# Performance work log

Measured on AMD Instinct MI355X. Metric: run time of the kernel, lower is better.

Reference implementation:

```python
import jax, jax.numpy as jnp
import numpy as np

# Layer geometry (matches init_kwargs): input_dims=[16,32,16] -> F=16 filters, S=32*16=512 shifts; O=32 output filters
F = 16
S = 512
O = 32
B = 256


def setup_inputs() -> dict:
    key = jax.random.key(0)
    k1, k2, k3 = jax.random.split(key, 3)
    x = jax.random.normal(k1, (B, S * F), dtype=jnp.float32)
    W = jax.random.normal(k2, (S * F, O), dtype=jnp.float32)
    b = jax.random.normal(k3, (O,), dtype=jnp.float32)
    return {"x": x, "W": W, "b": b}


def reference(x, W, b):
    # x: [B, S*F] -> [B, S, F]; W: [S*F, O] -> [S, F, O]
    xs = x.reshape(-1, S, F)
    w = W.reshape(S, F, O)
    # Contraction dim of the original tf.matmul is 1, so it is a broadcast
    # multiply producing a [B, S, F, O] intermediate.
    prod = xs[:, :, :, None] * w[None, :, :, :]   # [B, S, F, O]
    pre = jnp.sum(jnp.max(prod, axis=1), axis=1) + b  # max over shifts, sum over filters -> [B, O]
    return jax.nn.relu(pre)
```

## Files before the change

kernel.cpp:

```cpp
#include <hip/hip_runtime.h>

#define FDIM 16
#define SDIM 512
#define ODIM 32
#define SF   (SDIM * FDIM)
#define PAIRS 512
#define NB   8
#define SC   32
#define NSC  (SDIM / SC)
#define NBG  (256 / NB)

__global__ __launch_bounds__(256) void max_layer_phase1(
    const float* __restrict__ x, const float* __restrict__ W,
    float* __restrict__ part) {
  __shared__ float xs[NB * SC * FDIM];
  __shared__ float red[NB * PAIRS];

  const int t  = threadIdx.x;
  const int bg = blockIdx.x / NSC;
  const int sc = blockIdx.x % NSC;

  const float4* xin = (const float4*)x;
  float4* xs4 = (float4*)xs;
  for (int i = t; i < NB * SC * FDIM / 4; i += 256) {
    int b   = i / (SC * FDIM / 4);
    int off = i % (SC * FDIM / 4);
    xs4[i] = xin[(size_t)(bg * NB + b) * (SF / 4) + sc * (SC * FDIM / 4) + off];
  }
  __syncthreads();

  const int tq = t & 127;
  const int th = t >> 7;
  const int f  = tq >> 3;

  const float NEG = -3.402823466e+38f;
  float4 macc[NB];
#pragma unroll
  for (int b = 0; b < NB; ++b) macc[b] = make_float4(NEG, NEG, NEG, NEG);

  const float4* wp = (const float4*)W + (size_t)(sc * SC) * (PAIRS / 4) + tq;

#pragma unroll 4
  for (int j = 0; j < SC / 2; ++j) {
    const int s = th * (SC / 2) + j;
    float4 w = wp[s * (PAIRS / 4)];
    const float* xp = xs + s * FDIM + f;
#pragma unroll
    for (int b = 0; b < NB; ++b) {
      float xv = xp[b * SC * FDIM];
      macc[b].x = fmaxf(macc[b].x, xv * w.x);
      macc[b].y = fmaxf(macc[b].y, xv * w.y);
      macc[b].z = fmaxf(macc[b].z, xv * w.z);
      macc[b].w = fmaxf(macc[b].w, xv * w.w);
    }
  }

  if (th == 1) {
#pragma unroll
    for (int b = 0; b < NB; ++b) ((float4*)red)[b * 128 + tq] = macc[b];
  }
  __syncthreads();
  if (th == 0) {
#pragma unroll
    for (int b = 0; b < NB; ++b) {
      float4 o = ((float4*)red)[b * 128 + tq];
      o.x = fmaxf(o.x, macc[b].x);
      o.y = fmaxf(o.y, macc[b].y);
      o.z = fmaxf(o.z, macc[b].z);
      o.w = fmaxf(o.w, macc[b].w);
      ((float4*)part)[((size_t)(bg * NB + b) * NSC + sc) * (PAIRS / 4) + tq] = o;
    }
  }
}

__global__ __launch_bounds__(256) void max_layer_phase2(
    const float* __restrict__ part, const float* __restrict__ bias,
    float* __restrict__ out) {
  __shared__ float red[PAIRS];
  const int t = threadIdx.x;
  const int b = blockIdx.x;
  const float* pb = part + (size_t)b * NSC * PAIRS;
  for (int p = t; p < PAIRS; p += 256) {
    float m = pb[p];
#pragma unroll
    for (int c = 1; c < NSC; ++c) m = fmaxf(m, pb[c * PAIRS + p]);
    red[p] = m;
  }
  __syncthreads();
  if (t < ODIM) {
    float s = bias[t];
#pragma unroll
    for (int ff = 0; ff < FDIM; ++ff) s += red[ff * ODIM + t];
    out[b * ODIM + t] = fmaxf(s, 0.0f);
  }
}

extern "C" void kernel_launch(void* const* d_in, const int* in_sizes, int n_in,
                              void* d_out, int out_size, void* d_ws, size_t ws_size,
                              hipStream_t stream) {
  const float* x    = (const float*)d_in[0];
  const float* W    = (const float*)d_in[1];
  const float* bias = (const float*)d_in[2];
  float* out        = (float*)d_out;
  float* part       = (float*)d_ws;

  max_layer_phase1<<<dim3(NBG * NSC), dim3(256), 0, stream>>>(x, W, part);
  max_layer_phase2<<<dim3(256), dim3(256), 0, stream>>>(part, bias, out);
}
```

Baseline: 69.25 us.

## Fuse max-reduction phases into single kernel with per-block full shift sweep

Merges the two-kernel partial-max pipeline into one kernel where each block processes two batch rows over all shifts, splitting shifts across four thread slices and reducing in shared memory before summing filters and applying bias and ReLU. This removes the workspace round trip and the second launch. In exchange, grid size drops to 128 blocks and each block rereads all of W, raising W traffic and lowering parallelism.

```diff
diff --git a/kernel.cpp b/kernel.cpp
--- a/kernel.cpp
+++ b/kernel.cpp
@@ -5,27 +5,28 @@
 #define ODIM 32
 #define SF   (SDIM * FDIM)
 #define PAIRS 512
-#define NB   8
-#define SC   32
-#define NSC  (SDIM / SC)
-#define NBG  (256 / NB)
+#define NB   2
+#define NTH  512
+#define NSL  4
+#define SSL  (SDIM / NSL)
+#define NBLK (256 / NB)
 
-__global__ __launch_bounds__(256) void max_layer_phase1(
+__global__ __launch_bounds__(NTH) void max_layer_fused(
     const float* __restrict__ x, const float* __restrict__ W,
-    float* __restrict__ part) {
-  __shared__ float xs[NB * SC * FDIM];
-  __shared__ float red[NB * PAIRS];
+    const float* __restrict__ bias, float* __restrict__ out) {
+  __shared__ float  xs[NB * SF];
+  __shared__ float4 red[(NSL - 1) * NB * 128];
+  __shared__ float  redf[NB * PAIRS];
 
   const int t  = threadIdx.x;
-  const int bg = blockIdx.x / NSC;
-  const int sc = blockIdx.x % NSC;
+  const int b0 = blockIdx.x * NB;
 
-  const float4* xin = (const float4*)x;
+  const float4* xin = (const float4*)x + (size_t)b0 * (SF / 4);
   float4* xs4 = (float4*)xs;
-  for (int i = t; i < NB * SC * FDIM / 4; i += 256) {
-    int b   = i / (SC * FDIM / 4);
-    int off = i % (SC * FDIM / 4);
-    xs4[i] = xin[(size_t)(bg * NB + b) * (SF / 4) + sc * (SC * FDIM / 4) + off];
+#pragma unroll
+  for (int k = 0; k < NB * SF / 4 / NTH; ++k) {
+    const int i = t + k * NTH;
+    xs4[i] = xin[i];
   }
   __syncthreads();
 
@@ -38,16 +39,16 @@
 #pragma unroll
   for (int b = 0; b < NB; ++b) macc[b] = make_float4(NEG, NEG, NEG, NEG);
 
-  const float4* wp = (const float4*)W + (size_t)(sc * SC) * (PAIRS / 4) + tq;
+  const float4* wp = (const float4*)W + tq;
 
 #pragma unroll 4
-  for (int j = 0; j < SC / 2; ++j) {
-    const int s = th * (SC / 2) + j;
-    float4 w = wp[s * (PAIRS / 4)];
+  for (int j = 0; j < SSL; ++j) {
+    const int s = th * SSL + j;
+    float4 w = wp[(size_t)s * (PAIRS / 4)];
     const float* xp = xs + s * FDIM + f;
 #pragma unroll
     for (int b = 0; b < NB; ++b) {
-      float xv = xp[b * SC * FDIM];
+      float xv = xp[b * SF];
       macc[b].x = fmaxf(macc[b].x, xv * w.x);
       macc[b].y = fmaxf(macc[b].y, xv * w.y);
       macc[b].z = fmaxf(macc[b].z, xv * w.z);
@@ -55,43 +56,36 @@
     }
   }
 
-  if (th == 1) {
+  if (th >= 1) {
 #pragma unroll
-    for (int b = 0; b < NB; ++b) ((float4*)red)[b * 128 + tq] = macc[b];
+    for (int b = 0; b < NB; ++b)
+      red[((th - 1) * NB + b) * 128 + tq] = macc[b];
   }
   __syncthreads();
   if (th == 0) {
 #pragma unroll
     for (int b = 0; b < NB; ++b) {
-      float4 o = ((float4*)red)[b * 128 + tq];
-      o.x = fmaxf(o.x, macc[b].x);
-      o.y = fmaxf(o.y, macc[b].y);
-      o.z = fmaxf(o.z, macc[b].z);
-      o.w = fmaxf(o.w, macc[b].w);
-      ((float4*)part)[((size_t)(bg * NB + b) * NSC + sc) * (PAIRS / 4) + tq] = o;
+      float4 o = macc[b];
+#pragma unroll
+      for (int sl = 0; sl < NSL - 1; ++sl) {
+        float4 v = red[(sl * NB + b) * 128 + tq];
+        o.x = fmaxf(o.x, v.x);
+        o.y = fmaxf(o.y, v.y);
+        o.z = fmaxf(o.z, v.z);
+        o.w = fmaxf(o.w, v.w);
+      }
+      ((float4*)redf)[b * 128 + tq] = o;
     }
   }
-}
+  __syncthreads();
 
-__global__ __launch_bounds__(256) void max_layer_phase2(
-    const float* __restrict__ part, const float* __restrict__ bias,
-    float* __restrict__ out) {
-  __shared__ float red[PAIRS];
-  const int t = threadIdx.x;
-  const int b = blockIdx.x;
-  const float* pb = part + (size_t)b * NSC * PAIRS;
-  for (int p = t; p < PAIRS; p += 256) {
-    float m = pb[p];
+  if (t < NB * ODIM) {
+    const int b = t >> 5;
+    const int o = t & 31;
+    float s = bias[o];
 #pragma unroll
-    for (int c = 1; c < NSC; ++c) m = fmaxf(m, pb[c * PAIRS + p]);
-    red[p] = m;
-  }
-  __syncthreads();
-  if (t < ODIM) {
-    float s = bias[t];
-#pragma unroll
-    for (int ff = 0; ff < FDIM; ++ff) s += red[ff * ODIM + t];
-    out[b * ODIM + t] = fmaxf(s, 0.0f);
+    for (int ff = 0; ff < FDIM; ++ff) s += redf[b * PAIRS + ff * ODIM + o];
+    out[(size_t)(b0 + b) * ODIM + o] = fmaxf(s, 0.0f);
   }
 }
 
@@ -102,8 +96,7 @@
   const float* W    = (const float*)d_in[1];
   const float* bias = (const float*)d_in[2];
   float* out        = (float*)d_out;
-  float* part       = (float*)d_ws;
+  (void)d_ws; (void)ws_size;
 
-  max_layer_phase1<<<dim3(NBG * NSC), dim3(256), 0, stream>>>(x, W, part);
-  max_layer_phase2<<<dim3(256), dim3(256), 0, stream>>>(part, bias, out);
+  max_layer_fused<<<dim3(NBLK), dim3(NTH), 0, stream>>>(x, W, bias, out);
 }
```

Measured after the change: 73.96 us. 6.8% more time.
